# Kernel optimization log

Measured on AMD Instinct MI355X. Metric: run time of the kernel, lower is better.

The kernel has to match this reference:

```python
import jax, jax.numpy as jnp
import numpy as np

N = 100000   # nodes
E = 1600000  # directed edges (avg degree 16)
IN, HID, OUT = 32, 64, 32


def setup_inputs() -> dict:
    key = jax.random.key(0)
    k0, k1, k2, k3 = jax.random.split(key, 4)
    x = jax.random.normal(k0, (N, IN), dtype=jnp.float32)
    edge_index = jax.random.randint(k1, (2, E), 0, N, dtype=jnp.int32)
    W1 = jax.random.normal(k2, (IN, HID), dtype=jnp.float32) * (1.0 / np.sqrt(IN))
    b1 = jnp.zeros((HID,), dtype=jnp.float32)
    W2 = jax.random.normal(k3, (HID, OUT), dtype=jnp.float32) * (1.0 / np.sqrt(HID))
    b2 = jnp.zeros((OUT,), dtype=jnp.float32)
    return {"x": x, "edge_index": edge_index, "W1": W1, "b1": b1, "W2": W2, "b2": b2}


def gcn_conv(x, src, dst, W, b, n):
    # GCNConv: D^{-1/2} (A + I) D^{-1/2} X W + b, deg computed after self-loops
    h = x @ W                                   # [N, d_out]
    ones = jnp.ones_like(dst, dtype=h.dtype)
    deg = jax.ops.segment_sum(ones, dst, num_segments=n)   # >= 1 (self-loops)
    dinv = jax.lax.rsqrt(jnp.maximum(deg, 1.0))
    norm = dinv[src] * dinv[dst]                # [E + N]
    agg = jax.ops.segment_sum(norm[:, None] * h[src], dst, num_segments=n)
    return agg + b


def reference(x, edge_index, W1, b1, W2, b2):
    n = x.shape[0]
    loop = jnp.arange(n, dtype=edge_index.dtype)
    src = jnp.concatenate([edge_index[0], loop])  # add self-loops once
    dst = jnp.concatenate([edge_index[1], loop])
    h = jax.nn.relu(gcn_conv(x, src, dst, W1, b1, n))
    # dropout omitted (eval mode)
    out = gcn_conv(h, src, dst, W2, b2, n)
    return out
```

## Files before the change

### kernel.cpp

```cpp
#include <hip/hip_runtime.h>
#include <stdint.h>

#define IN_F  32
#define HID_F 64
#define OUT_F 32

#define BKT_SHIFT 8
#define BKT_NODES 256
#define NBLK      512

__device__ inline unsigned short f2bf(float f) {
    unsigned u = __float_as_uint(f);
    return (unsigned short)((u + 0x7FFF + ((u >> 16) & 1)) >> 16);
}
__device__ inline float bflo(unsigned w) { return __uint_as_float(w << 16); }
__device__ inline float bfhi(unsigned w) { return __uint_as_float(w & 0xFFFF0000u); }


__global__ __launch_bounds__(256) void count_kernel(const int* __restrict__ dst,
                                                    int* __restrict__ cnt, int E, int nb)
{
    __shared__ int hist[1024];
    int tid = threadIdx.x;
    for (int i = tid; i < nb; i += 256) hist[i] = 0;
    __syncthreads();
    for (int e = blockIdx.x * 256 + tid; e < E; e += NBLK * 256)
        atomicAdd(&hist[dst[e] >> BKT_SHIFT], 1);
    __syncthreads();
    for (int i = tid; i < nb; i += 256) cnt[i * NBLK + blockIdx.x] = hist[i];
}

__global__ __launch_bounds__(NBLK) void bsum_kernel(const int* __restrict__ cnt,
                                                    int* __restrict__ bsum)
{
    __shared__ int s[NBLK];
    int tid = threadIdx.x, b = blockIdx.x;
    s[tid] = cnt[b * NBLK + tid];
    __syncthreads();
    for (int off = NBLK / 2; off > 0; off >>= 1) {
        if (tid < off) s[tid] += s[tid + off];
        __syncthreads();
    }
    if (tid == 0) bsum[b] = s[0];
}

__global__ __launch_bounds__(512) void bscan_kernel(int* __restrict__ bsum, int nb,
                                                    int* __restrict__ cellstart, int nc,
                                                    int* __restrict__ rowstart, int n, int E)
{
    __shared__ int s[512];
    int tid = threadIdx.x;
    int my = (tid < nb) ? bsum[tid] : 0;
    s[tid] = my;
    __syncthreads();
    for (int off = 1; off < 512; off <<= 1) {
        int t = (tid >= off) ? s[tid - off] : 0;
        __syncthreads();
        s[tid] += t;
        __syncthreads();
    }
    if (tid < nb) bsum[tid] = s[tid] - my;
    if (tid == 0) { cellstart[nc] = E; rowstart[n] = E; }
}

__global__ __launch_bounds__(NBLK) void cscan_kernel(const int* __restrict__ cnt,
                                                     const int* __restrict__ bsum,
                                                     int* __restrict__ cellstart)
{
    __shared__ int s[NBLK];
    int tid = threadIdx.x, b = blockIdx.x;
    int my = cnt[b * NBLK + tid];
    s[tid] = my;
    __syncthreads();
    for (int off = 1; off < NBLK; off <<= 1) {
        int t = (tid >= off) ? s[tid - off] : 0;
        __syncthreads();
        s[tid] += t;
        __syncthreads();
    }
    cellstart[b * NBLK + tid] = bsum[b] + s[tid] - my;
}

__global__ __launch_bounds__(256) void append_kernel(
    const int* __restrict__ src, const int* __restrict__ dst,
    const int* __restrict__ cellstart, unsigned* __restrict__ pairs, int E, int nb)
{
    __shared__ int cur[1024];
    int tid = threadIdx.x;
    for (int i = tid; i < nb; i += 256) cur[i] = cellstart[i * NBLK + blockIdx.x];
    __syncthreads();
    for (int e = blockIdx.x * 256 + tid; e < E; e += NBLK * 256) {
        int d = dst[e];
        int pos = atomicAdd(&cur[d >> BKT_SHIFT], 1);
        pairs[pos] = ((unsigned)src[e] << BKT_SHIFT) | (unsigned)(d & (BKT_NODES - 1));
    }
}

__global__ __launch_bounds__(256) void place_kernel(
    const int* __restrict__ cellstart, const unsigned* __restrict__ pairs,
    int* __restrict__ srcs, int* __restrict__ rowstart, float* __restrict__ dinv,
    const float* __restrict__ x, unsigned* __restrict__ xs2, int n)
{
    __shared__ int hist[BKT_NODES];
    __shared__ int ofs[BKT_NODES];
    __shared__ float sdv[BKT_NODES];
    int b = blockIdx.x, tid = threadIdx.x;
    int beg = cellstart[b * NBLK], end = cellstart[(b + 1) * NBLK];
    hist[tid] = 0;
    __syncthreads();
    for (int e = beg + tid; e < end; e += 256)
        atomicAdd(&hist[pairs[e] & (BKT_NODES - 1)], 1);
    __syncthreads();
    int my = hist[tid];
    ofs[tid] = my;
    __syncthreads();
    for (int off = 1; off < 256; off <<= 1) {
        int t = (tid >= off) ? ofs[tid - off] : 0;
        __syncthreads();
        ofs[tid] += t;
        __syncthreads();
    }
    int excl = ofs[tid] - my;
    int node = b * BKT_NODES + tid;
    float dv = rsqrtf((float)(my + 1));
    sdv[tid] = dv;
    if (node < n) {
        rowstart[node] = beg + excl;
        dinv[node] = dv;
    }
    __syncthreads();
    ofs[tid] = excl;
    __syncthreads();
    for (int e = beg + tid; e < end; e += 256) {
        unsigned p = pairs[e];
        int dl = p & (BKT_NODES - 1);
        int pos = beg + atomicAdd(&ofs[dl], 1);
        srcs[pos] = (int)(p >> BKT_SHIFT);
    }
    int base = b * BKT_NODES;
    for (int idx = tid; idx < BKT_NODES * (IN_F / 2); idx += 256) {
        int nl = idx >> 4;
        int p  = idx & 15;
        int nd = base + nl;
        if (nd < n) {
            float2 v = ((const float2*)x)[((size_t)nd << 4) + p];
            float d = sdv[nl];
            unsigned pack = (unsigned)f2bf(v.x * d) | ((unsigned)f2bf(v.y * d) << 16);
            xs2[((size_t)nd << 4) + p] = pack;
        }
    }
}

__global__ __launch_bounds__(256) void fused1_kernel(
    const int* __restrict__ rowstart, const int* __restrict__ srcs,
    const unsigned* __restrict__ xs2, const float* __restrict__ dinv,
    const float* __restrict__ b1, const float* __restrict__ W1,
    const float* __restrict__ W2, unsigned* __restrict__ hs2p, int n)
{
    __shared__ float W1s[IN_F * HID_F];
    __shared__ float W2s[HID_F * OUT_F];
    __shared__ float grow[16][IN_F + 1];
    __shared__ float hrow[16][HID_F + 1];
    int tid = threadIdx.x;
    for (int t = tid; t < IN_F * HID_F; t += 256) W1s[t] = W1[t];
    for (int t = tid; t < HID_F * OUT_F; t += 256) W2s[t] = W2[t];

    int nl = tid >> 4;
    unsigned q = tid & 15;
    int node = blockIdx.x * 16 + nl;
    bool active = node < n;
    int nodec = active ? node : 0;

    int beg = rowstart[nodec], end = active ? rowstart[nodec + 1] : beg;
    unsigned ws = active ? xs2[((unsigned)nodec << 4) + q] : 0u;
    float a0l = bflo(ws), a0h = bfhi(ws);
    float a1l = 0.f, a1h = 0.f, a2l = 0.f, a2h = 0.f, a3l = 0.f, a3h = 0.f;
    float a4l = 0.f, a4h = 0.f, a5l = 0.f, a5h = 0.f, a6l = 0.f, a6h = 0.f;
    float a7l = 0.f, a7h = 0.f;
    int e = beg;
    for (; e + 8 <= end; e += 8) {
        unsigned o0 = ((unsigned)srcs[e]     << 4) + q, o1 = ((unsigned)srcs[e + 1] << 4) + q;
        unsigned o2 = ((unsigned)srcs[e + 2] << 4) + q, o3 = ((unsigned)srcs[e + 3] << 4) + q;
        unsigned o4 = ((unsigned)srcs[e + 4] << 4) + q, o5 = ((unsigned)srcs[e + 5] << 4) + q;
        unsigned o6 = ((unsigned)srcs[e + 6] << 4) + q, o7 = ((unsigned)srcs[e + 7] << 4) + q;
        unsigned w0 = xs2[o0], w1 = xs2[o1], w2 = xs2[o2], w3 = xs2[o3];
        unsigned w4 = xs2[o4], w5 = xs2[o5], w6 = xs2[o6], w7 = xs2[o7];
        a0l += bflo(w0); a0h += bfhi(w0); a1l += bflo(w1); a1h += bfhi(w1);
        a2l += bflo(w2); a2h += bfhi(w2); a3l += bflo(w3); a3h += bfhi(w3);
        a4l += bflo(w4); a4h += bfhi(w4); a5l += bflo(w5); a5h += bfhi(w5);
        a6l += bflo(w6); a6h += bfhi(w6); a7l += bflo(w7); a7h += bfhi(w7);
    }
    for (; e + 4 <= end; e += 4) {
        unsigned o0 = ((unsigned)srcs[e]     << 4) + q, o1 = ((unsigned)srcs[e + 1] << 4) + q;
        unsigned o2 = ((unsigned)srcs[e + 2] << 4) + q, o3 = ((unsigned)srcs[e + 3] << 4) + q;
        unsigned w0 = xs2[o0], w1 = xs2[o1], w2 = xs2[o2], w3 = xs2[o3];
        a0l += bflo(w0); a0h += bfhi(w0); a1l += bflo(w1); a1h += bfhi(w1);
        a2l += bflo(w2); a2h += bfhi(w2); a3l += bflo(w3); a3h += bfhi(w3);
    }
    for (; e < end; ++e) {
        unsigned w0 = xs2[((unsigned)srcs[e] << 4) + q];
        a0l += bflo(w0); a0h += bfhi(w0);
    }
    float dv = dinv[nodec];
    grow[nl][2 * q]     = dv * (((a0l + a1l) + (a2l + a3l)) + ((a4l + a5l) + (a6l + a7l)));
    grow[nl][2 * q + 1] = dv * (((a0h + a1h) + (a2h + a3h)) + ((a4h + a5h) + (a6h + a7h)));
    __syncthreads();

    float h0 = b1[q], h1 = b1[q + 16], h2 = b1[q + 32], h3 = b1[q + 48];
    #pragma unroll
    for (int k = 0; k < IN_F; ++k) {
        float gk = grow[nl][k];
        h0 += gk * W1s[k * HID_F + q];
        h1 += gk * W1s[k * HID_F + q + 16];
        h2 += gk * W1s[k * HID_F + q + 32];
        h3 += gk * W1s[k * HID_F + q + 48];
    }
    hrow[nl][q]      = fmaxf(h0, 0.f);
    hrow[nl][q + 16] = fmaxf(h1, 0.f);
    hrow[nl][q + 32] = fmaxf(h2, 0.f);
    hrow[nl][q + 48] = fmaxf(h3, 0.f);
    __syncthreads();

    float p0 = 0.f, p1 = 0.f;
    #pragma unroll
    for (int k = 0; k < HID_F; ++k) {
        float hk = hrow[nl][k];
        p0 += hk * W2s[k * OUT_F + 2 * q];
        p1 += hk * W2s[k * OUT_F + 2 * q + 1];
    }
    if (active) {
        unsigned pack = (unsigned)f2bf(dv * p0) | ((unsigned)f2bf(dv * p1) << 16);
        hs2p[((unsigned)node << 4) + q] = pack;
    }
}

__global__ __launch_bounds__(256) void agg2_kernel(
    const int* __restrict__ rowstart, const int* __restrict__ srcs,
    const uint2* __restrict__ hs2p2, const float* __restrict__ dinv,
    const float* __restrict__ b2, float* __restrict__ out, int n)
{
    int t = blockIdx.x * blockDim.x + threadIdx.x;
    int node = t >> 3;
    if (node >= n) return;
    unsigned r = t & 7;
    int beg = rowstart[node], end = rowstart[node + 1];
    uint2 ws = hs2p2[((unsigned)node << 3) + r];
    float a0x = bflo(ws.x), a0y = bfhi(ws.x), a0z = bflo(ws.y), a0w = bfhi(ws.y);
    float a1x = 0.f, a1y = 0.f, a1z = 0.f, a1w = 0.f;
    float a2x = 0.f, a2y = 0.f, a2z = 0.f, a2w = 0.f;
    float a3x = 0.f, a3y = 0.f, a3z = 0.f, a3w = 0.f;
    int e = beg;
    for (; e + 4 <= end; e += 4) {
        unsigned o0 = ((unsigned)srcs[e]     << 3) + r, o1 = ((unsigned)srcs[e + 1] << 3) + r;
        unsigned o2 = ((unsigned)srcs[e + 2] << 3) + r, o3 = ((unsigned)srcs[e + 3] << 3) + r;
        uint2 w0 = hs2p2[o0], w1 = hs2p2[o1], w2 = hs2p2[o2], w3 = hs2p2[o3];
        a0x += bflo(w0.x); a0y += bfhi(w0.x); a0z += bflo(w0.y); a0w += bfhi(w0.y);
        a1x += bflo(w1.x); a1y += bfhi(w1.x); a1z += bflo(w1.y); a1w += bfhi(w1.y);
        a2x += bflo(w2.x); a2y += bfhi(w2.x); a2z += bflo(w2.y); a2w += bfhi(w2.y);
        a3x += bflo(w3.x); a3y += bfhi(w3.x); a3z += bflo(w3.y); a3w += bfhi(w3.y);
    }
    for (; e < end; ++e) {
        uint2 w0 = hs2p2[((unsigned)srcs[e] << 3) + r];
        a0x += bflo(w0.x); a0y += bfhi(w0.x); a0z += bflo(w0.y); a0w += bfhi(w0.y);
    }
    float dvv = dinv[node];
    float4 bb = ((const float4*)b2)[r];
    float4 res;
    res.x = dvv * ((a0x + a1x) + (a2x + a3x)) + bb.x;
    res.y = dvv * ((a0y + a1y) + (a2y + a3y)) + bb.y;
    res.z = dvv * ((a0z + a1z) + (a2z + a3z)) + bb.z;
    res.w = dvv * ((a0w + a1w) + (a2w + a3w)) + bb.w;
    ((float4*)out)[((size_t)node << 3) + r] = res;
}

extern "C" void kernel_launch(void* const* d_in, const int* in_sizes, int n_in,
                              void* d_out, int out_size, void* d_ws, size_t ws_size,
                              hipStream_t stream) {
    const float* x  = (const float*)d_in[0];
    const int*   ei = (const int*)  d_in[1];
    const float* W1 = (const float*)d_in[2];
    const float* b1 = (const float*)d_in[3];
    const float* W2 = (const float*)d_in[4];
    const float* b2 = (const float*)d_in[5];
    float* out = (float*)d_out;

    const int n = in_sizes[0] / IN_F;
    const int E = in_sizes[1] / 2;
    const int* src = ei;
    const int* dst = ei + E;

    const int nb = (n + BKT_NODES - 1) >> BKT_SHIFT;
    const int nc = nb * NBLK;

    auto align16 = [](int* p) { return (int*)(((uintptr_t)p + 15) & ~(uintptr_t)15); };
    int* ip = (int*)d_ws;
    int* cnt       = ip;                 ip += nc;
    int* cellstart = ip;                 ip += nc + 1;
    int* bsum      = ip;                 ip += nb + 1;
    int* rowstart  = ip;                 ip += n + 1;
    ip = align16(ip);
    unsigned* pairs = (unsigned*)ip;     ip += E;
    int* srcs_srt  = ip;                 ip += E;
    float* dinv = (float*)ip;            ip += n;
    ip = align16(ip);
    unsigned* xs2  = (unsigned*)ip;      ip += (size_t)n * IN_F / 2;
    ip = align16(ip);
    unsigned* hs2p = (unsigned*)ip;

    count_kernel<<<NBLK, 256, 0, stream>>>(dst, cnt, E, nb);
    bsum_kernel <<<nb, NBLK, 0, stream>>>(cnt, bsum);
    bscan_kernel<<<1, 512, 0, stream>>>(bsum, nb, cellstart, nc, rowstart, n, E);
    cscan_kernel<<<nb, NBLK, 0, stream>>>(cnt, bsum, cellstart);
    append_kernel<<<NBLK, 256, 0, stream>>>(src, dst, cellstart, pairs, E, nb);
    place_kernel<<<nb, 256, 0, stream>>>(cellstart, pairs, srcs_srt, rowstart, dinv, x, xs2, n);

    fused1_kernel<<<(n + 15) / 16, 256, 0, stream>>>(rowstart, srcs_srt, xs2, dinv, b1, W1, W2, hs2p, n);
    agg2_kernel<<<((size_t)n * 8 + 255) / 256, 256, 0, stream>>>(rowstart, srcs_srt, (const uint2*)hs2p, dinv, b2, out, n);
}
```

Before: 214.0 us.

## Fuse CSR preprocessing kernels into one cooperative kernel with grid syncs

New measurement: 409.5 us. +91.4%, slower.

```diff
diff --git a/kernel.cpp b/kernel.cpp
--- a/kernel.cpp
+++ b/kernel.cpp
@@ -1,5 +1,8 @@
 #include <hip/hip_runtime.h>
+#include <hip/hip_cooperative_groups.h>
 #include <stdint.h>
+
+namespace cg = cooperative_groups;
 
 #define IN_F  32
 #define HID_F 64
@@ -16,6 +19,141 @@
 __device__ inline float bflo(unsigned w) { return __uint_as_float(w << 16); }
 __device__ inline float bfhi(unsigned w) { return __uint_as_float(w & 0xFFFF0000u); }
 
+
+__device__ inline void scan512_excl(int* s, int* sums, int tid) {
+    int a = s[2 * tid], b = s[2 * tid + 1];
+    int ts = a + b;
+    sums[tid] = ts;
+    __syncthreads();
+    #pragma unroll
+    for (int off = 1; off < 256; off <<= 1) {
+        int t = (tid >= off) ? sums[tid - off] : 0;
+        __syncthreads();
+        sums[tid] += t;
+        __syncthreads();
+    }
+    int texcl = sums[tid] - ts;
+    s[2 * tid]     = texcl;
+    s[2 * tid + 1] = texcl + a;
+    __syncthreads();
+}
+
+__global__ __launch_bounds__(256) void prep_kernel(
+    const int* __restrict__ src, const int* __restrict__ dst,
+    int* __restrict__ cnt, int* __restrict__ btot, int* __restrict__ cellx,
+    unsigned* __restrict__ pairs, int* __restrict__ srcs,
+    int* __restrict__ rowstart, float* __restrict__ dinv,
+    const float* __restrict__ x, unsigned* __restrict__ xs2,
+    int E, int n, int nb)
+{
+    __shared__ int sA[1024];
+    __shared__ int sB[512];
+    __shared__ int sS[256];
+    cg::grid_group grid = cg::this_grid();
+    int tid = threadIdx.x, blk = blockIdx.x;
+
+    for (int i = tid; i < nb; i += 256) sA[i] = 0;
+    __syncthreads();
+    for (int e = blk * 256 + tid; e < E; e += NBLK * 256)
+        atomicAdd(&sA[dst[e] >> BKT_SHIFT], 1);
+    __syncthreads();
+    for (int i = tid; i < nb; i += 256) cnt[i * NBLK + blk] = sA[i];
+
+    grid.sync();
+
+    if (blk < nb) {
+        int c0 = cnt[blk * NBLK + 2 * tid];
+        int c1 = cnt[blk * NBLK + 2 * tid + 1];
+        int ps = c0 + c1;
+        sS[tid] = ps;
+        __syncthreads();
+        #pragma unroll
+        for (int off = 1; off < 256; off <<= 1) {
+            int t = (tid >= off) ? sS[tid - off] : 0;
+            __syncthreads();
+            sS[tid] += t;
+            __syncthreads();
+        }
+        int incl = sS[tid], excl = incl - ps;
+        cellx[blk * NBLK + 2 * tid]     = excl;
+        cellx[blk * NBLK + 2 * tid + 1] = excl + c0;
+        if (tid == 255) btot[blk] = incl;
+    }
+
+    grid.sync();
+
+    sB[tid]       = (tid < nb)       ? btot[tid]       : 0;
+    sB[256 + tid] = (256 + tid < nb) ? btot[256 + tid] : 0;
+    __syncthreads();
+    scan512_excl(sB, sS, tid);
+    for (int i = tid; i < nb; i += 256) sA[i] = sB[i] + cellx[i * NBLK + blk];
+    __syncthreads();
+    for (int e = blk * 256 + tid; e < E; e += NBLK * 256) {
+        int d = dst[e];
+        int pos = atomicAdd(&sA[d >> BKT_SHIFT], 1);
+        pairs[pos] = ((unsigned)src[e] << BKT_SHIFT) | (unsigned)(d & (BKT_NODES - 1));
+    }
+
+    grid.sync();
+
+    if (blk < nb) {
+        sB[tid]       = (tid < nb)       ? btot[tid]       : 0;
+        sB[256 + tid] = (256 + tid < nb) ? btot[256 + tid] : 0;
+        __syncthreads();
+        scan512_excl(sB, sS, tid);
+        int beg = sB[blk];
+        int end = beg + btot[blk];
+        int* hist = sA;
+        int* ofs  = sA + 256;
+        float* sdv = (float*)sS;
+
+        hist[tid] = 0;
+        __syncthreads();
+        for (int e = beg + tid; e < end; e += 256)
+            atomicAdd(&hist[pairs[e] & (BKT_NODES - 1)], 1);
+        __syncthreads();
+        int my = hist[tid];
+        ofs[tid] = my;
+        __syncthreads();
+        #pragma unroll
+        for (int off = 1; off < 256; off <<= 1) {
+            int t = (tid >= off) ? ofs[tid - off] : 0;
+            __syncthreads();
+            ofs[tid] += t;
+            __syncthreads();
+        }
+        int excl = ofs[tid] - my;
+        int node = blk * BKT_NODES + tid;
+        float dv = rsqrtf((float)(my + 1));
+        sdv[tid] = dv;
+        if (node < n) {
+            rowstart[node] = beg + excl;
+            dinv[node] = dv;
+        }
+        __syncthreads();
+        ofs[tid] = excl;
+        __syncthreads();
+        for (int e = beg + tid; e < end; e += 256) {
+            unsigned p = pairs[e];
+            int dl = p & (BKT_NODES - 1);
+            int pos = beg + atomicAdd(&ofs[dl], 1);
+            srcs[pos] = (int)(p >> BKT_SHIFT);
+        }
+        int base = blk * BKT_NODES;
+        for (int idx = tid; idx < BKT_NODES * (IN_F / 2); idx += 256) {
+            int nl = idx >> 4;
+            int p  = idx & 15;
+            int nd = base + nl;
+            if (nd < n) {
+                float2 v = ((const float2*)x)[((size_t)nd << 4) + p];
+                float d = sdv[nl];
+                unsigned pack = (unsigned)f2bf(v.x * d) | ((unsigned)f2bf(v.y * d) << 16);
+                xs2[((size_t)nd << 4) + p] = pack;
+            }
+        }
+        if (blk == 0 && tid == 0) rowstart[n] = E;
+    }
+}
 
 __global__ __launch_bounds__(256) void count_kernel(const int* __restrict__ dst,
                                                     int* __restrict__ cnt, int E, int nb)
@@ -284,19 +422,19 @@
     const float* b2 = (const float*)d_in[5];
     float* out = (float*)d_out;
 
-    const int n = in_sizes[0] / IN_F;
-    const int E = in_sizes[1] / 2;
+    int n = in_sizes[0] / IN_F;
+    int E = in_sizes[1] / 2;
     const int* src = ei;
     const int* dst = ei + E;
 
-    const int nb = (n + BKT_NODES - 1) >> BKT_SHIFT;
+    int nb = (n + BKT_NODES - 1) >> BKT_SHIFT;
     const int nc = nb * NBLK;
 
     auto align16 = [](int* p) { return (int*)(((uintptr_t)p + 15) & ~(uintptr_t)15); };
     int* ip = (int*)d_ws;
     int* cnt       = ip;                 ip += nc;
-    int* cellstart = ip;                 ip += nc + 1;
-    int* bsum      = ip;                 ip += nb + 1;
+    int* cellx     = ip;                 ip += nc + 1;
+    int* btot      = ip;                 ip += nb + 1;
     int* rowstart  = ip;                 ip += n + 1;
     ip = align16(ip);
     unsigned* pairs = (unsigned*)ip;     ip += E;
@@ -307,12 +445,20 @@
     ip = align16(ip);
     unsigned* hs2p = (unsigned*)ip;
 
-    count_kernel<<<NBLK, 256, 0, stream>>>(dst, cnt, E, nb);
-    bsum_kernel <<<nb, NBLK, 0, stream>>>(cnt, bsum);
-    bscan_kernel<<<1, 512, 0, stream>>>(bsum, nb, cellstart, nc, rowstart, n, E);
-    cscan_kernel<<<nb, NBLK, 0, stream>>>(cnt, bsum, cellstart);
-    append_kernel<<<NBLK, 256, 0, stream>>>(src, dst, cellstart, pairs, E, nb);
-    place_kernel<<<nb, 256, 0, stream>>>(cellstart, pairs, srcs_srt, rowstart, dinv, x, xs2, n);
+    void* kargs[] = { (void*)&src, (void*)&dst, (void*)&cnt, (void*)&btot, (void*)&cellx,
+                      (void*)&pairs, (void*)&srcs_srt, (void*)&rowstart, (void*)&dinv,
+                      (void*)&x, (void*)&xs2, (void*)&E, (void*)&n, (void*)&nb };
+    hipError_t ce = hipLaunchCooperativeKernel((void*)prep_kernel, dim3(NBLK), dim3(256),
+                                               kargs, 0, stream);
+    if (ce != hipSuccess) {
+        (void)hipGetLastError();
+        count_kernel<<<NBLK, 256, 0, stream>>>(dst, cnt, E, nb);
+        bsum_kernel <<<nb, NBLK, 0, stream>>>(cnt, btot);
+        bscan_kernel<<<1, 512, 0, stream>>>(btot, nb, cellx, nc, rowstart, n, E);
+        cscan_kernel<<<nb, NBLK, 0, stream>>>(cnt, btot, cellx);
+        append_kernel<<<NBLK, 256, 0, stream>>>(src, dst, cellx, pairs, E, nb);
+        place_kernel<<<nb, 256, 0, stream>>>(cellx, pairs, srcs_srt, rowstart, dinv, x, xs2, n);
+    }
 
     fused1_kernel<<<(n + 15) / 16, 256, 0, stream>>>(rowstart, srcs_srt, xs2, dinv, b1, W1, W2, hs2p, n);
     agg2_kernel<<<((size_t)n * 8 + 255) / 256, 256, 0, stream>>>(rowstart, srcs_srt, (const uint2*)hs2p, dinv, b2, out, n);
```
